# Performance work log

Measured on AMD Instinct MI355X. Metric: run time of the kernel, lower is better.

The kernel has to match this reference:

```python
import jax, jax.numpy as jnp
import numpy as np
from math import pi, sqrt, factorial

NUM_SPHERICAL = 7
NUM_RADIAL = 6
CUTOFF = 5.0
ENV_P = 6  # envelope_exponent + 1
E_EDGES = 300000
T_TRIPLETS = 600000

# ---- static numpy precompute: spherical-Bessel zeros + normalizers (DimeNet bessel_basis) ----

def _jn_np(x, n):
    x = np.asarray(x, dtype=np.float64)
    j0 = np.sin(x) / x
    if n == 0:
        return j0
    jm, j = j0, np.sin(x) / x ** 2 - np.cos(x) / x
    for l in range(2, n + 1):
        jm, j = j, (2 * l - 1) / x * j - jm
    return j

def _bessel_zeros(n, k):
    total = k + n - 1
    zeros = np.zeros((n, total))
    zeros[0, :] = np.arange(1, total + 1) * np.pi
    for l in range(1, n):
        for i in range(total - l):
            a, b = zeros[l - 1, i], zeros[l - 1, i + 1]
            fa = _jn_np(a, l)
            for _ in range(80):  # bisection; zeros of j_l interlace zeros of j_{l-1}
                m = 0.5 * (a + b)
                fm = _jn_np(m, l)
                if fa * fm <= 0:
                    b = m
                else:
                    a, fa = m, fm
            zeros[l, i] = 0.5 * (a + b)
    return zeros[:, :k]

_Z = _bessel_zeros(NUM_SPHERICAL, NUM_RADIAL)  # [n, k] zeros z_{l,i}
_NORM = np.stack([1.0 / np.sqrt(0.5 * _jn_np(_Z[l], l + 1) ** 2) for l in range(NUM_SPHERICAL)])
_Z_J = jnp.asarray(_Z, jnp.float32)
_NORM_J = jnp.asarray(_NORM, jnp.float32)

# ---- jnp basis evaluation ----

def _sph_jl(x, l):
    # spherical Bessel j_l via upward recurrence (same closed sin/cos form as sympy lambdify)
    j0 = jnp.sin(x) / x
    if l == 0:
        return j0
    jm, j = j0, jnp.sin(x) / x ** 2 - jnp.cos(x) / x
    for ll in range(2, l + 1):
        jm, j = j, (2 * ll - 1) / x * j - jm
    return j

def _rbf(dist_scaled):
    # [E] -> [E, n, k]; row l = norm_{l,i} * j_l(z_{l,i} * x)
    rows = [_NORM_J[l] * _sph_jl(dist_scaled[:, None] * _Z_J[l], l) for l in range(NUM_SPHERICAL)]
    return jnp.stack(rows, axis=1)

def _assoc_legendre(cost, sint, lmax):
    # Condon-Shortley associated Legendre P_l^m(cos theta), sint = sin(theta) >= 0
    P = {(0, 0): jnp.ones_like(cost)}
    for m in range(1, lmax + 1):
        P[(m, m)] = (1 - 2 * m) * P[(m - 1, m - 1)] * sint
    for m in range(0, lmax):
        P[(m + 1, m)] = (2 * m + 1) * cost * P[(m, m)]
    for m in range(0, lmax + 1):
        for l in range(m + 2, lmax + 1):
            P[(l, m)] = ((2 * l - 1) * cost * P[(l - 1, m)] - (l + m - 1) * P[(l - 2, m)]) / (l - m)
    return P

def _cbf_angle(angle):
    # zero_m_only real spherical harmonics Y_l^0(theta); l=0 column is the constant Y_0^0
    P = _assoc_legendre(jnp.cos(angle), jnp.sin(angle), NUM_SPHERICAL - 1)
    cols = [jnp.full_like(angle, 0.5 / sqrt(pi))]
    for l in range(1, NUM_SPHERICAL):
        cols.append(sqrt((2 * l + 1) / (4.0 * pi)) * P[(l, 0)])
    return jnp.stack(cols, axis=1)  # [T, n]

def _cbf_torsion(angle, phi):
    # full real spherical harmonics, flat order: Y00, then per l: m=-l..l (sin, m=0, cos)
    P = _assoc_legendre(jnp.cos(angle), jnp.sin(angle), NUM_SPHERICAL - 1)
    cols = [jnp.full_like(angle, 0.5 / sqrt(pi))]
    for l in range(1, NUM_SPHERICAL):
        for m in range(-l, l + 1):
            am = abs(m)
            K = sqrt((2 * l + 1) / (4.0 * pi) * factorial(l - am) / factorial(l + am))
            if m < 0:
                cols.append(sqrt(2.0) * K * jnp.sin(am * phi) * P[(l, am)])
            elif m == 0:
                cols.append(K * P[(l, 0)])
            else:
                cols.append(sqrt(2.0) * K * jnp.cos(m * phi) * P[(l, m)])
    return jnp.stack(cols, axis=1)  # [T, n*n]

def setup_inputs() -> dict:
    key = jax.random.key(0)
    k1, k2, k3, k4 = jax.random.split(key, 4)
    dist = jax.random.uniform(k1, (E_EDGES,), jnp.float32, 0.5, CUTOFF)
    angle = jax.random.uniform(k2, (T_TRIPLETS,), jnp.float32, 0.0, pi)
    torsion = jax.random.uniform(k3, (T_TRIPLETS,), jnp.float32, -pi, pi)
    idx_kj = jax.random.randint(k4, (T_TRIPLETS,), 0, E_EDGES, jnp.int32)
    freq = jnp.arange(1, NUM_RADIAL + 1, dtype=jnp.float32) * pi  # DitanceEmbedding param init
    return {"dist": dist, "angle": angle, "torsion": torsion, "freq": freq, "idx_kj": idx_kj}

def reference(dist, angle, torsion, freq, idx_kj):
    n, k = NUM_SPHERICAL, NUM_RADIAL
    p = ENV_P
    a = -(p + 1) * (p + 2) / 2.0   # -28
    b = float(p * (p + 2))         # 48
    c = -p * (p + 1) / 2.0         # -21
    # DitanceEmbedding: envelope(x) * sin(freq * x)
    x = (dist / CUTOFF)[:, None]
    xp0 = x ** (p - 1)
    env = 1.0 / x + a * xp0 + b * xp0 * x + c * xp0 * x * x
    dist_emb = env * jnp.sin(freq * x)                      # [E, k]
    # shared radial basis on scaled dist
    rbf = _rbf(dist / CUTOFF)                               # [E, n, k]
    rbf_g = rbf[idx_kj]                                     # [T, n, k] gather per triplet
    # AngleEmbedding
    cbf_a = _cbf_angle(angle)                               # [T, n]
    angle_emb = (rbf_g * cbf_a[:, :, None]).reshape(-1, n * k)
    # TorsionEmbedding
    cbf_t = _cbf_torsion(angle, torsion).reshape(-1, n, n, 1)
    torsion_emb = (rbf_g[:, None, :, :] * cbf_t).reshape(-1, n * n * k)
    return (dist_emb, angle_emb, torsion_emb)
```

## Files before the change

kernel.cpp:

```cpp
#include <hip/hip_runtime.h>

#define NS 7
#define NK 6
#define TW 294
#define TPB 32

typedef float f4 __attribute__((ext_vector_type(4)));

__constant__ float ZG[6][6] = {
    {4.4934095f, 7.7252518f, 10.9041217f, 14.0661939f, 17.2207553f, 20.3713030f},
    {5.7634592f, 9.0950113f, 12.3229410f, 15.5146030f, 18.6890364f, 21.8538742f},
    {6.9879320f, 10.4171185f, 13.6980232f, 16.9236213f, 20.1218062f, 23.3042470f},
    {8.1825615f, 11.7049072f, 15.0396647f, 18.3012560f, 21.5254177f, 24.7275655f},
    {9.3558121f, 12.9665302f, 16.3547096f, 19.6531521f, 22.9045506f, 26.1277501f},
    {10.5128354f, 14.2073925f, 17.6479743f, 20.9834631f, 24.2627681f, 27.5078684f}
};

__device__ __forceinline__ void jl_pair(float x, int l, float* jlm1, float* jl) {
    float s = sinf(x), c = cosf(x);
    float inv = 1.0f / x;
    float jm = c * inv;
    float j = s * inv;
    for (int ll = 1; ll <= l; ++ll) {
        float t = (float)(2 * ll - 1) * inv * j - jm;
        jm = j;
        j = t;
    }
    *jlm1 = jm;
    *jl = j;
}

__launch_bounds__(256, 8)
__global__ void fused_kernel(const float* __restrict__ dist,
                             const float* __restrict__ angle,
                             const float* __restrict__ torsion,
                             const float* __restrict__ freq,
                             const int* __restrict__ idx_kj,
                             float* __restrict__ outD,
                             float* __restrict__ outA,
                             float* __restrict__ outT,
                             int E, int T, int NBT) {
    __shared__ __align__(16) float smem[3112];
    const int tid = threadIdx.x;

    if (blockIdx.x >= NBT) {
        const int e0 = (blockIdx.x - NBT) * 256;
        int e = e0 + tid;
        int ec = e < E ? e : E - 1;
        float x = dist[ec] * 0.2f;
        float inv = 1.0f / x;
        float x2 = x * x;
        float xp0 = x2 * x2 * x;
        float env = inv - 28.0f * xp0 + 48.0f * xp0 * x - 21.0f * xp0 * x2;
        float v[NK];
        #pragma unroll
        for (int i = 0; i < NK; ++i) v[i] = env * __sinf(freq[i] * x);
        if (e0 + 256 <= E) {
            #pragma unroll
            for (int i = 0; i < NK; ++i) smem[tid * 6 + i] = v[i];
            __syncthreads();
            const f4* b4 = (const f4*)smem;
            f4* o4 = (f4*)(outD + (size_t)e0 * 6);
            __builtin_nontemporal_store(b4[tid], o4 + tid);
            if (tid < 128) __builtin_nontemporal_store(b4[256 + tid], o4 + 256 + tid);
        } else if (e < E) {
            #pragma unroll
            for (int i = 0; i < NK; ++i) outD[(size_t)e * 6 + i] = v[i];
        }
        return;
    }

    float* __restrict__ rbf_s = smem;
    float* __restrict__ cbf_s = smem + 1408;
    float* __restrict__ zc    = smem + 2976;
    float* __restrict__ nc    = smem + 3018;
    float* __restrict__ Kc    = smem + 3060;

    if (tid < 42) {
        int l = tid / 6, i = tid - 6 * l;
        if (l == 0) {
            float z = (float)(i + 1) * 3.14159265358979f;
            zc[tid] = z;
            nc[tid] = z * 1.41421356237309f;
        } else {
            float x = ZG[l - 1][i];
            #pragma unroll
            for (int it = 0; it < 4; ++it) {
                float jm, jv;
                jl_pair(x, l, &jm, &jv);
                float d = jm - (float)(l + 1) / x * jv;
                x -= jv / d;
            }
            float jm, jv;
            jl_pair(x, l, &jm, &jv);
            float jn1 = (float)(2 * l + 1) / x * jv - jm;
            zc[tid] = x;
            nc[tid] = 1.41421356237309f / fabsf(jn1);
        }
    } else if (tid >= 64 && tid < 113) {
        int f = tid - 64;
        int l = 0;
        while ((l + 1) * (l + 1) <= f) ++l;
        int m = f - l * l - l;
        int am = m < 0 ? -m : m;
        float ratio = 1.0f;
        for (int t = l - am + 1; t <= l + am; ++t) ratio /= (float)t;
        float K = sqrtf((float)(2 * l + 1) * 0.07957747154594767f * ratio);
        if (m != 0) K *= 1.41421356237309505f;
        Kc[f] = K;
    }
    const int t0 = blockIdx.x * TPB;
    __syncthreads();

    if (tid < TPB) {
        int t = t0 + tid;
        int tc = t < T ? t : T - 1;
        float ang = angle[tc];
        float phi = torsion[tc];

        float st = __sinf(ang), ct = __cosf(ang);
        float sp = __sinf(phi), cp = __cosf(phi);
        float sm[NS], cm[NS];
        sm[1] = sp; cm[1] = cp;
        #pragma unroll
        for (int m = 2; m < NS; ++m) {
            sm[m] = sm[m - 1] * cp + cm[m - 1] * sp;
            cm[m] = cm[m - 1] * cp - sm[m - 1] * sp;
        }

        float* cb = cbf_s + tid * 49;
        float pmm = 1.0f;
        #pragma unroll
        for (int m = 0; m < NS; ++m) {
            if (m > 0) pmm = (float)(1 - 2 * m) * pmm * st;
            {
                int f = m * m + m;
                if (m == 0) cb[f] = Kc[f];
                else {
                    cb[f + m] = Kc[f + m] * cm[m] * pmm;
                    cb[f - m] = Kc[f - m] * sm[m] * pmm;
                }
            }
            if (m < NS - 1) {
                float plm1 = pmm;
                float pl = (float)(2 * m + 1) * ct * pmm;
                {
                    int l = m + 1, f = l * l + l;
                    if (m == 0) cb[f] = Kc[f] * pl;
                    else {
                        cb[f + m] = Kc[f + m] * cm[m] * pl;
                        cb[f - m] = Kc[f - m] * sm[m] * pl;
                    }
                }
                #pragma unroll
                for (int l = m + 2; l < NS; ++l) {
                    float pn = ((float)(2 * l - 1) * ct * pl -
                                (float)(l + m - 1) * plm1) / (float)(l - m);
                    plm1 = pl; pl = pn;
                    int f = l * l + l;
                    if (m == 0) cb[f] = Kc[f] * pl;
                    else {
                        cb[f + m] = Kc[f + m] * cm[m] * pl;
                        cb[f - m] = Kc[f - m] * sm[m] * pl;
                    }
                }
            }
        }
    } else if (tid >= 64 && tid < 64 + 6 * TPB) {
        int w = tid - 64;
        int s = w / 6, p = w - 6 * s;
        int t = t0 + s;
        int tc = t < T ? t : T - 1;
        int idx = idx_kj[tc];
        float x = dist[idx] * 0.2f;
        int jlo = p * 7;
        for (int jj = jlo; jj < jlo + 7; ++jj) {
            int l = jj / 6;
            float arg = zc[jj] * x;
            float s1 = __sinf(arg), c1 = __cosf(arg);
            float inv = 1.0f / arg;
            float j0 = s1 * inv;
            float val = j0;
            if (l >= 1) {
                float jm = j0;
                float jcur = (s1 * inv - c1) * inv;
                for (int ll = 2; ll <= l; ++ll) {
                    float tmp = (float)(2 * ll - 1) * inv * jcur - jm;
                    jm = jcur;
                    jcur = tmp;
                }
                val = jcur;
            }
            rbf_s[s * 44 + jj] = nc[jj] * val;
        }
    }
    __syncthreads();

    int nvalid = T - t0; if (nvalid > TPB) nvalid = TPB;

    if (nvalid == TPB) {
        f4* __restrict__ gT = (f4*)(outT + (size_t)t0 * TW);
        unsigned row = (unsigned)(4 * tid) / 294u;
        unsigned c   = (unsigned)(4 * tid) - row * 294u;
        #pragma unroll
        for (int it = 0; it < 10; ++it) {
            if (it < 9 || tid < 48) {
                unsigned row1 = row, c1 = c + 2;
                if (c1 >= 294u) { c1 -= 294u; row1 += 1; }
                unsigned a0 = c / 42u,  r0 = c - a0 * 42u,  q0 = a0 * 7u + r0 / 6u;
                unsigned a1 = c1 / 42u, r1 = c1 - a1 * 42u, q1 = a1 * 7u + r1 / 6u;
                float qv0 = cbf_s[row * 49 + q0];
                float2 rv0 = *(const float2*)&rbf_s[row * 44 + r0];
                float qv1 = cbf_s[row1 * 49 + q1];
                float2 rv1 = *(const float2*)&rbf_s[row1 * 44 + r1];
                f4 val = { qv0 * rv0.x, qv0 * rv0.y, qv1 * rv1.x, qv1 * rv1.y };
                __builtin_nontemporal_store(val, gT + it * 256 + tid);
            }
            c += 142u; row += 3u;
            if (c >= 294u) { c -= 294u; row += 1u; }
        }
        f4* __restrict__ gA = (f4*)(outA + (size_t)t0 * 42);
        unsigned arow = (unsigned)(4 * tid) / 42u;
        unsigned ac   = (unsigned)(4 * tid) - arow * 42u;
        #pragma unroll
        for (int it = 0; it < 2; ++it) {
            if (it < 1 || tid < 80) {
                unsigned arow1 = arow, ac1 = ac + 2;
                if (ac1 >= 42u) { ac1 -= 42u; arow1 += 1; }
                unsigned l0 = ac / 6u,  qa0 = l0 * l0 + l0;
                unsigned l1 = ac1 / 6u, qa1 = l1 * l1 + l1;
                float qv0 = cbf_s[arow * 49 + qa0];
                float2 rv0 = *(const float2*)&rbf_s[arow * 44 + ac];
                float qv1 = cbf_s[arow1 * 49 + qa1];
                float2 rv1 = *(const float2*)&rbf_s[arow1 * 44 + ac1];
                f4 val = { qv0 * rv0.x, qv0 * rv0.y, qv1 * rv1.x, qv1 * rv1.y };
                __builtin_nontemporal_store(val, gA + it * 256 + tid);
            }
            ac += 16u; arow += 24u;
            if (ac >= 42u) { ac -= 42u; arow += 1u; }
        }
    } else {
        for (int g = tid; g < nvalid * TW; g += 256) {
            int row = g / TW, cc = g - row * TW;
            int a = cc / 42, r = cc - a * 42;
            outT[(size_t)t0 * TW + g] = cbf_s[row * 49 + a * 7 + r / 6] * rbf_s[row * 44 + r];
        }
        for (int g = tid; g < nvalid * 42; g += 256) {
            int row = g / 42, r = g - row * 42;
            int l = r / 6;
            outA[(size_t)t0 * 42 + g] = cbf_s[row * 49 + l * l + l] * rbf_s[row * 44 + r];
        }
    }
}

extern "C" void kernel_launch(void* const* d_in, const int* in_sizes, int n_in,
                              void* d_out, int out_size, void* d_ws, size_t ws_size,
                              hipStream_t stream) {
    const float* dist    = (const float*)d_in[0];
    const float* angle   = (const float*)d_in[1];
    const float* torsion = (const float*)d_in[2];
    const float* freq    = (const float*)d_in[3];
    const int*   idx_kj  = (const int*)d_in[4];
    const int E = in_sizes[0];
    const int T = in_sizes[1];
    float* out = (float*)d_out;
    float* outA = out + (size_t)E * NK;
    float* outT = outA + (size_t)T * 42;

    const int NBT = (T + TPB - 1) / TPB;
    const int NBD = (E + 255) / 256;
    fused_kernel<<<NBT + NBD, 256, 0, stream>>>(dist, angle, torsion, freq, idx_kj,
                                                out, outA, outT, E, T, NBT);
}
```

Measured before the change: 159.0 us.

## Process four triplet tiles per block with double-buffered LDS compute/store overlap

Each triplet block now handles four 32-triplet tiles, with two LDS buffers so the next tile's basis computation can overlap the current tile's global stores. The per-block constant setup (Bessel zeros, normalizers, spherical-harmonic constants) is amortized over four tiles, and the Newton refinement of the zeros is dropped in favor of the tabulated values with fast sin/cos. Launch bounds drop to 4 waves-occupancy hint and LDS use nearly doubles, which lowers occupancy, and skipping the refinement may slightly change the accuracy of the normalizers.

```diff
diff --git a/kernel.cpp b/kernel.cpp
--- a/kernel.cpp
+++ b/kernel.cpp
@@ -4,6 +4,7 @@
 #define NK 6
 #define TW 294
 #define TPB 32
+#define NTILES 4
 
 typedef float f4 __attribute__((ext_vector_type(4)));
 
@@ -16,8 +17,8 @@
     {10.5128354f, 14.2073925f, 17.6479743f, 20.9834631f, 24.2627681f, 27.5078684f}
 };
 
-__device__ __forceinline__ void jl_pair(float x, int l, float* jlm1, float* jl) {
-    float s = sinf(x), c = cosf(x);
+__device__ __forceinline__ void jl_pair_fast(float x, int l, float* jlm1, float* jl) {
+    float s = __sinf(x), c = __cosf(x);
     float inv = 1.0f / x;
     float jm = c * inv;
     float j = s * inv;
@@ -30,88 +31,14 @@
     *jl = j;
 }
 
-__launch_bounds__(256, 8)
-__global__ void fused_kernel(const float* __restrict__ dist,
-                             const float* __restrict__ angle,
-                             const float* __restrict__ torsion,
-                             const float* __restrict__ freq,
-                             const int* __restrict__ idx_kj,
-                             float* __restrict__ outD,
-                             float* __restrict__ outA,
-                             float* __restrict__ outT,
-                             int E, int T, int NBT) {
-    __shared__ __align__(16) float smem[3112];
-    const int tid = threadIdx.x;
-
-    if (blockIdx.x >= NBT) {
-        const int e0 = (blockIdx.x - NBT) * 256;
-        int e = e0 + tid;
-        int ec = e < E ? e : E - 1;
-        float x = dist[ec] * 0.2f;
-        float inv = 1.0f / x;
-        float x2 = x * x;
-        float xp0 = x2 * x2 * x;
-        float env = inv - 28.0f * xp0 + 48.0f * xp0 * x - 21.0f * xp0 * x2;
-        float v[NK];
-        #pragma unroll
-        for (int i = 0; i < NK; ++i) v[i] = env * __sinf(freq[i] * x);
-        if (e0 + 256 <= E) {
-            #pragma unroll
-            for (int i = 0; i < NK; ++i) smem[tid * 6 + i] = v[i];
-            __syncthreads();
-            const f4* b4 = (const f4*)smem;
-            f4* o4 = (f4*)(outD + (size_t)e0 * 6);
-            __builtin_nontemporal_store(b4[tid], o4 + tid);
-            if (tid < 128) __builtin_nontemporal_store(b4[256 + tid], o4 + 256 + tid);
-        } else if (e < E) {
-            #pragma unroll
-            for (int i = 0; i < NK; ++i) outD[(size_t)e * 6 + i] = v[i];
-        }
-        return;
-    }
-
-    float* __restrict__ rbf_s = smem;
-    float* __restrict__ cbf_s = smem + 1408;
-    float* __restrict__ zc    = smem + 2976;
-    float* __restrict__ nc    = smem + 3018;
-    float* __restrict__ Kc    = smem + 3060;
-
-    if (tid < 42) {
-        int l = tid / 6, i = tid - 6 * l;
-        if (l == 0) {
-            float z = (float)(i + 1) * 3.14159265358979f;
-            zc[tid] = z;
-            nc[tid] = z * 1.41421356237309f;
-        } else {
-            float x = ZG[l - 1][i];
-            #pragma unroll
-            for (int it = 0; it < 4; ++it) {
-                float jm, jv;
-                jl_pair(x, l, &jm, &jv);
-                float d = jm - (float)(l + 1) / x * jv;
-                x -= jv / d;
-            }
-            float jm, jv;
-            jl_pair(x, l, &jm, &jv);
-            float jn1 = (float)(2 * l + 1) / x * jv - jm;
-            zc[tid] = x;
-            nc[tid] = 1.41421356237309f / fabsf(jn1);
-        }
-    } else if (tid >= 64 && tid < 113) {
-        int f = tid - 64;
-        int l = 0;
-        while ((l + 1) * (l + 1) <= f) ++l;
-        int m = f - l * l - l;
-        int am = m < 0 ? -m : m;
-        float ratio = 1.0f;
-        for (int t = l - am + 1; t <= l + am; ++t) ratio /= (float)t;
-        float K = sqrtf((float)(2 * l + 1) * 0.07957747154594767f * ratio);
-        if (m != 0) K *= 1.41421356237309505f;
-        Kc[f] = K;
-    }
-    const int t0 = blockIdx.x * TPB;
-    __syncthreads();
-
+__device__ __forceinline__ void compute_tile(
+    int t0, int T,
+    const float* __restrict__ angle, const float* __restrict__ torsion,
+    const float* __restrict__ dist, const int* __restrict__ idx_kj,
+    const float* __restrict__ zc, const float* __restrict__ nc,
+    const float* __restrict__ Kc,
+    float* __restrict__ rbf, float* __restrict__ cbf, int tid)
+{
     if (tid < TPB) {
         int t = t0 + tid;
         int tc = t < T ? t : T - 1;
@@ -128,7 +55,7 @@
             cm[m] = cm[m - 1] * cp - sm[m - 1] * sp;
         }
 
-        float* cb = cbf_s + tid * 49;
+        float* cb = cbf + tid * 49;
         float pmm = 1.0f;
         #pragma unroll
         for (int m = 0; m < NS; ++m) {
@@ -191,13 +118,16 @@
                 }
                 val = jcur;
             }
-            rbf_s[s * 44 + jj] = nc[jj] * val;
-        }
-    }
-    __syncthreads();
-
+            rbf[s * 44 + jj] = nc[jj] * val;
+        }
+    }
+}
+
+__device__ __forceinline__ void store_tile(
+    int t0, int T, const float* __restrict__ rbf, const float* __restrict__ cbf,
+    float* __restrict__ outA, float* __restrict__ outT, int tid)
+{
     int nvalid = T - t0; if (nvalid > TPB) nvalid = TPB;
-
     if (nvalid == TPB) {
         f4* __restrict__ gT = (f4*)(outT + (size_t)t0 * TW);
         unsigned row = (unsigned)(4 * tid) / 294u;
@@ -209,10 +139,10 @@
                 if (c1 >= 294u) { c1 -= 294u; row1 += 1; }
                 unsigned a0 = c / 42u,  r0 = c - a0 * 42u,  q0 = a0 * 7u + r0 / 6u;
                 unsigned a1 = c1 / 42u, r1 = c1 - a1 * 42u, q1 = a1 * 7u + r1 / 6u;
-                float qv0 = cbf_s[row * 49 + q0];
-                float2 rv0 = *(const float2*)&rbf_s[row * 44 + r0];
-                float qv1 = cbf_s[row1 * 49 + q1];
-                float2 rv1 = *(const float2*)&rbf_s[row1 * 44 + r1];
+                float qv0 = cbf[row * 49 + q0];
+                float2 rv0 = *(const float2*)&rbf[row * 44 + r0];
+                float qv1 = cbf[row1 * 49 + q1];
+                float2 rv1 = *(const float2*)&rbf[row1 * 44 + r1];
                 f4 val = { qv0 * rv0.x, qv0 * rv0.y, qv1 * rv1.x, qv1 * rv1.y };
                 __builtin_nontemporal_store(val, gT + it * 256 + tid);
             }
@@ -229,10 +159,10 @@
                 if (ac1 >= 42u) { ac1 -= 42u; arow1 += 1; }
                 unsigned l0 = ac / 6u,  qa0 = l0 * l0 + l0;
                 unsigned l1 = ac1 / 6u, qa1 = l1 * l1 + l1;
-                float qv0 = cbf_s[arow * 49 + qa0];
-                float2 rv0 = *(const float2*)&rbf_s[arow * 44 + ac];
-                float qv1 = cbf_s[arow1 * 49 + qa1];
-                float2 rv1 = *(const float2*)&rbf_s[arow1 * 44 + ac1];
+                float qv0 = cbf[arow * 49 + qa0];
+                float2 rv0 = *(const float2*)&rbf[arow * 44 + ac];
+                float qv1 = cbf[arow1 * 49 + qa1];
+                float2 rv1 = *(const float2*)&rbf[arow1 * 44 + ac1];
                 f4 val = { qv0 * rv0.x, qv0 * rv0.y, qv1 * rv1.x, qv1 * rv1.y };
                 __builtin_nontemporal_store(val, gA + it * 256 + tid);
             }
@@ -243,13 +173,98 @@
         for (int g = tid; g < nvalid * TW; g += 256) {
             int row = g / TW, cc = g - row * TW;
             int a = cc / 42, r = cc - a * 42;
-            outT[(size_t)t0 * TW + g] = cbf_s[row * 49 + a * 7 + r / 6] * rbf_s[row * 44 + r];
+            outT[(size_t)t0 * TW + g] = cbf[row * 49 + a * 7 + r / 6] * rbf[row * 44 + r];
         }
         for (int g = tid; g < nvalid * 42; g += 256) {
             int row = g / 42, r = g - row * 42;
             int l = r / 6;
-            outA[(size_t)t0 * 42 + g] = cbf_s[row * 49 + l * l + l] * rbf_s[row * 44 + r];
-        }
+            outA[(size_t)t0 * 42 + g] = cbf[row * 49 + l * l + l] * rbf[row * 44 + r];
+        }
+    }
+}
+
+__launch_bounds__(256, 4)
+__global__ void fused_kernel(const float* __restrict__ dist,
+                             const float* __restrict__ angle,
+                             const float* __restrict__ torsion,
+                             const float* __restrict__ freq,
+                             const int* __restrict__ idx_kj,
+                             float* __restrict__ outD,
+                             float* __restrict__ outA,
+                             float* __restrict__ outT,
+                             int E, int T, int NBLK_T, int NBTILES) {
+    __shared__ __align__(16) float smem[2 * 2976 + 133];
+    const int tid = threadIdx.x;
+
+    if (blockIdx.x >= NBLK_T) {
+        const int e0 = (blockIdx.x - NBLK_T) * 256;
+        int e = e0 + tid;
+        int ec = e < E ? e : E - 1;
+        float x = dist[ec] * 0.2f;
+        float inv = 1.0f / x;
+        float x2 = x * x;
+        float xp0 = x2 * x2 * x;
+        float env = inv - 28.0f * xp0 + 48.0f * xp0 * x - 21.0f * xp0 * x2;
+        float v[NK];
+        #pragma unroll
+        for (int i = 0; i < NK; ++i) v[i] = env * __sinf(freq[i] * x);
+        if (e0 + 256 <= E) {
+            #pragma unroll
+            for (int i = 0; i < NK; ++i) smem[tid * 6 + i] = v[i];
+            __syncthreads();
+            const f4* b4 = (const f4*)smem;
+            f4* o4 = (f4*)(outD + (size_t)e0 * 6);
+            __builtin_nontemporal_store(b4[tid], o4 + tid);
+            if (tid < 128) __builtin_nontemporal_store(b4[256 + tid], o4 + 256 + tid);
+        } else if (e < E) {
+            #pragma unroll
+            for (int i = 0; i < NK; ++i) outD[(size_t)e * 6 + i] = v[i];
+        }
+        return;
+    }
+
+    float* buf0 = smem;
+    float* buf1 = smem + 2976;
+    float* zc = smem + 5952;
+    float* nc = zc + 42;
+    float* Kc = nc + 42;
+
+    if (tid < 42) {
+        int l = tid / 6, i = tid - 6 * l;
+        float z = (l == 0) ? (float)(i + 1) * 3.14159265358979f : ZG[l - 1][i];
+        float jm, jv;
+        jl_pair_fast(z, l + 1, &jm, &jv);
+        zc[tid] = z;
+        nc[tid] = 1.41421356237309f / fabsf(jv);
+    } else if (tid >= 64 && tid < 113) {
+        int f = tid - 64;
+        int l = 0;
+        while ((l + 1) * (l + 1) <= f) ++l;
+        int m = f - l * l - l;
+        int am = m < 0 ? -m : m;
+        float ratio = 1.0f;
+        for (int t = l - am + 1; t <= l + am; ++t) ratio /= (float)t;
+        float K = sqrtf((float)(2 * l + 1) * 0.07957747154594767f * ratio);
+        if (m != 0) K *= 1.41421356237309505f;
+        Kc[f] = K;
+    }
+    const int tilebase = blockIdx.x * NTILES;
+    __syncthreads();
+
+    compute_tile(tilebase * TPB, T, angle, torsion, dist, idx_kj,
+                 zc, nc, Kc, buf0, buf0 + 1408, tid);
+    __syncthreads();
+
+    for (int k = 0; k < NTILES; ++k) {
+        int tile = tilebase + k;
+        if (tile >= NBTILES) break;
+        float* bc = (k & 1) ? buf1 : buf0;
+        float* bn = (k & 1) ? buf0 : buf1;
+        store_tile(tile * TPB, T, bc, bc + 1408, outA, outT, tid);
+        if (k + 1 < NTILES && tile + 1 < NBTILES)
+            compute_tile((tile + 1) * TPB, T, angle, torsion, dist, idx_kj,
+                         zc, nc, Kc, bn, bn + 1408, tid);
+        __syncthreads();
     }
 }
 
@@ -267,8 +282,9 @@
     float* outA = out + (size_t)E * NK;
     float* outT = outA + (size_t)T * 42;
 
-    const int NBT = (T + TPB - 1) / TPB;
+    const int NBTILES = (T + TPB - 1) / TPB;
+    const int NBLK_T = (NBTILES + NTILES - 1) / NTILES;
     const int NBD = (E + 255) / 256;
-    fused_kernel<<<NBT + NBD, 256, 0, stream>>>(dist, angle, torsion, freq, idx_kj,
-                                                out, outA, outT, E, T, NBT);
-}
+    fused_kernel<<<NBLK_T + NBD, 256, 0, stream>>>(dist, angle, torsion, freq, idx_kj,
+                                                   out, outA, outT, E, T, NBLK_T, NBTILES);
+}
```

After: 296.7 us. 1.87x slower.
